# Kernel tuning notes

Measured on AMD Instinct MI355X. Metric: run time of the kernel, lower is better.

## Reference

```python
import jax, jax.numpy as jnp
import numpy as np

B, S, H = 4, 2048, 1024
NH = 1                     # source code only type-checks with 1 head (see notes)
DH = H // NH               # head dim == hidden size
DT = 32                    # distance_type
LN_EPS = 1e-12


def setup_inputs() -> dict:
    key = jax.random.key(0)
    ks = jax.random.split(key, 12)
    sd = 0.02
    hidden_states = jax.random.normal(ks[0], (B, S, H), dtype=jnp.float32)
    attention_mask = jnp.zeros((B, 1, 1, S), dtype=jnp.float32)
    word_word_relation = jax.random.randint(ks[1], (B, S, S), 0, DT, dtype=jnp.int64)
    dist_emb = sd * jax.random.normal(ks[2], (DT, H), dtype=jnp.float32)
    dist_emb = dist_emb.at[0].set(0.0)  # padding_idx=0
    return {
        "hidden_states": hidden_states,
        "attention_mask": attention_mask,
        "word_word_relation": word_word_relation,
        "Wq": sd * jax.random.normal(ks[3], (H, H), dtype=jnp.float32),
        "bq": jnp.zeros((H,), dtype=jnp.float32),
        "Wk": sd * jax.random.normal(ks[4], (H, H), dtype=jnp.float32),
        "bk": jnp.zeros((H,), dtype=jnp.float32),
        "Wv": sd * jax.random.normal(ks[5], (H, H), dtype=jnp.float32),
        "bv": jnp.zeros((H,), dtype=jnp.float32),
        "dist_emb": dist_emb,
        "Wo": sd * jax.random.normal(ks[6], (H, H), dtype=jnp.float32),
        "bo": jnp.zeros((H,), dtype=jnp.float32),
        "ln_g": jnp.ones((H,), dtype=jnp.float32),
        "ln_b": jnp.zeros((H,), dtype=jnp.float32),
    }


def _split_heads(x):
    # [B,S,H] -> [B,NH,S,DH]
    return x.reshape(B, S, NH, DH).transpose(0, 2, 1, 3)


def reference(hidden_states, attention_mask, word_word_relation, Wq, bq, Wk, bk,
              Wv, bv, dist_emb, Wo, bo, ln_g, ln_b):
    q = _split_heads(hidden_states @ Wq.T + bq)   # [B,NH,S,DH]
    k = _split_heads(hidden_states @ Wk.T + bk)
    v = _split_heads(hidden_states @ Wv.T + bv)

    # raw QK^T scores [B,NH,S,S]
    scores = jnp.einsum('bhqd,bhkd->bhqk', q, k)

    # query . distance_embedding^T : [B,NH,S,DT]
    word_dot_distance = jnp.einsum('bhqd,td->bhqt', q, dist_emb)

    rel = word_word_relation[:, None, :, :]       # [B,1,S,S]
    # gather per-pair distance score along the distance-type axis
    dist_att = jnp.take_along_axis(word_dot_distance, rel, axis=3)  # [B,NH,S,S]
    mask_out = (rel == 1).astype(scores.dtype)    # keep only relation==1 pairs
    dist_att = dist_att * mask_out

    scores = (scores + dist_att) / jnp.sqrt(jnp.asarray(DH, scores.dtype))
    scores = scores + attention_mask              # additive BERT mask
    probs = jax.nn.softmax(scores, axis=-1)       # dropout p=0 -> identity

    ctx = jnp.einsum('bhqk,bhkd->bhqd', probs, v) # [B,NH,S,DH]
    ctx = ctx.transpose(0, 2, 1, 3).reshape(B, S, H)

    # BertSelfOutput: dense -> residual -> LayerNorm
    attn_out = ctx @ Wo.T + bo
    x = attn_out + hidden_states
    mu = jnp.mean(x, axis=-1, keepdims=True)
    var = jnp.mean(jnp.square(x - mu), axis=-1, keepdims=True)
    out = (x - mu) * jax.lax.rsqrt(var + LN_EPS) * ln_g + ln_b
    return out
```

## Files before the change

### kernel.cpp

```cpp
#include <hip/hip_runtime.h>

#define BM 256
#define BN 128
#define BK 64
#define NBUF 3
#define BUFELEMS ((BM + BN) * BK)

typedef __bf16 bf16x8 __attribute__((ext_vector_type(8)));
typedef __bf16 bf16x4 __attribute__((ext_vector_type(4)));
typedef float f32x4 __attribute__((ext_vector_type(4)));
typedef __bf16 bf16_t;

#define MFMA16(a, b, c) __builtin_amdgcn_mfma_f32_16x16x32_bf16((a), (b), (c), 0, 0, 0)

__device__ __forceinline__ void gl_lds16(const void* g, void* l) {
    __builtin_amdgcn_global_load_lds(
        (const __attribute__((address_space(1))) void*)g,
        (__attribute__((address_space(3))) void*)l, 16, 0, 0);
}
__device__ __forceinline__ void barrier_mem() {
    asm volatile("s_barrier" ::: "memory");
}

__global__ __launch_bounds__(256)
void cvt_all_kernel(const float* __restrict__ hid,
                    const float* __restrict__ w0, const float* __restrict__ w1,
                    const float* __restrict__ w2, const float* __restrict__ w3,
                    bf16_t* __restrict__ hidb, bf16_t* __restrict__ wb)
{
    const int bid = blockIdx.x;
    const float* src;
    bf16_t* dst;
    size_t off;
    if (bid < 8192) {
        src = hid; dst = hidb; off = (size_t)bid * 1024;
    } else {
        const int i = (bid - 8192) >> 10;
        src = (i == 0) ? w0 : (i == 1) ? w1 : (i == 2) ? w2 : w3;
        dst = wb + (size_t)i * 1024 * 1024;
        off = (size_t)((bid - 8192) & 1023) * 1024;
    }
    const size_t idx = off + threadIdx.x * 4;
    const float4 v = *(const float4*)(src + idx);
    bf16x4 o;
    o[0] = (__bf16)v.x; o[1] = (__bf16)v.y;
    o[2] = (__bf16)v.z; o[3] = (__bf16)v.w;
    *(bf16x4*)(dst + idx) = o;
}

#define PHASE(BUF, P, SG, SL, VM)                                            \
  do {                                                                       \
    bf16x8 a00 = rdA(BUF, 2 * (P), 0),     a01 = rdA(BUF, 2 * (P), 1);       \
    bf16x8 a10 = rdA(BUF, 2 * (P) + 1, 0), a11 = rdA(BUF, 2 * (P) + 1, 1);   \
    if ((P) == 0) {                                                          \
      _Pragma("unroll")                                                      \
      for (int nf = 0; nf < 4; ++nf) {                                       \
        bfrag[nf][0] = rdB(BUF, nf, 0);                                      \
        bfrag[nf][1] = rdB(BUF, nf, 1);                                      \
      }                                                                      \
    }                                                                        \
    if (SG) {                                                                \
      gl_lds16((SG) + soff,                   (SL) + (w << 9));              \
      gl_lds16((SG) + soff + (size_t)64 * K,  (SL) + 4096 + (w << 9));       \
    }                                                                        \
    barrier_mem();                                                           \
    asm volatile("s_waitcnt lgkmcnt(0)" ::: "memory");                       \
    __builtin_amdgcn_s_setprio(1);                                           \
    _Pragma("unroll")                                                        \
    for (int nf = 0; nf < 4; ++nf) {                                         \
      acc[2 * (P)][nf]     = MFMA16(a00, bfrag[nf][0], acc[2 * (P)][nf]);    \
      acc[2 * (P)][nf]     = MFMA16(a01, bfrag[nf][1], acc[2 * (P)][nf]);    \
      acc[2 * (P) + 1][nf] = MFMA16(a10, bfrag[nf][0], acc[2 * (P) + 1][nf]);\
      acc[2 * (P) + 1][nf] = MFMA16(a11, bfrag[nf][1], acc[2 * (P) + 1][nf]);\
    }                                                                        \
    __builtin_amdgcn_s_setprio(0);                                           \
    if ((VM) == 4)      asm volatile("s_waitcnt vmcnt(4)" ::: "memory");     \
    else if ((VM) == 0) asm volatile("s_waitcnt vmcnt(0)" ::: "memory");     \
    barrier_mem();                                                           \
  } while (0)

template <int MODE>
__global__ __launch_bounds__(512, 2)
void gemm8(const bf16_t* __restrict__ A, const bf16_t* __restrict__ Bw,
           const float* __restrict__ bias, const float* __restrict__ bias2,
           const float* __restrict__ bias3,
           bf16_t* __restrict__ C, bf16_t* __restrict__ C2,
           int M, int N, int K,
           long long sAz, long long sBz, long long sCz,
           int Sdim, int DHdim)
{
    const int bz = blockIdx.z;
    const float* bi = bias;
    if (MODE == 0) {
        Bw += (long long)bz * N * K;
        bi = (bz == 0) ? bias : (bz == 1 ? bias2 : bias3);
        if (bz < 2) C += (long long)bz * sCz;
    } else {
        A += (long long)bz * sAz;
        Bw += (long long)bz * sBz;
        C += (long long)bz * sCz;
    }
    const int num_n = N >> 8;
    const int pid = blockIdx.x;
    const int group = 8 * num_n;
    const int g = pid / group;
    const int m0 = (g * 8 + (pid % 8)) * 256;
    const int n0 = ((pid % group) >> 3) * 256;

    const int tid = threadIdx.x;
    const int w = tid >> 6;
    const int lane = tid & 63;
    const int wr = w >> 2;
    const int wc = w & 3;
    const int frow = lane & 15;
    const int fchunk = lane >> 4;

    __shared__ bf16_t smem[4 * 16384];
    bf16_t* A0b = smem;
    bf16_t* A1b = smem + 16384;
    bf16_t* B0b = smem + 32768;
    bf16_t* B1b = smem + 49152;

    const int srow = tid >> 3;
    const int sch  = (tid & 7) ^ (srow & 7);
    const size_t soff = (size_t)srow * K + ((size_t)sch << 3);

    const bf16_t* gA = A + (size_t)m0 * K;
    const bf16_t* gB = Bw + (size_t)n0 * K;

    auto rdA = [&](int buf, int mf, int kh) -> bf16x8 {
        const int row = wr * 128 + mf * 16 + frow;
        return *(const bf16x8*)&smem[buf * 16384 + row * 64 +
                                     (((kh * 4 + fchunk) ^ (frow & 7)) << 3)];
    };
    auto rdB = [&](int buf, int nf, int kh) -> bf16x8 {
        const int row = wc * 64 + nf * 16 + frow;
        return *(const bf16x8*)&smem[32768 + buf * 16384 + row * 64 +
                                     (((kh * 4 + fchunk) ^ (frow & 7)) << 3)];
    };
    auto issue = [&](const bf16_t* sg, bf16_t* sl) {
        gl_lds16(sg + soff,                  sl + (w << 9));
        gl_lds16(sg + soff + (size_t)64 * K, sl + 4096 + (w << 9));
    };

    f32x4 acc[8][4];
#pragma unroll
    for (int i = 0; i < 8; ++i)
#pragma unroll
        for (int j = 0; j < 4; ++j) acc[i][j] = (f32x4)0.0f;
    bf16x8 bfrag[4][2];

    const int NT = K >> 6;
    const int NI = NT >> 1;

    issue(gB,                       B0b);
    issue(gB + (size_t)128 * K,     B0b + 8192);
    issue(gA,                       A0b);
    issue(gA + (size_t)128 * K,     A0b + 8192);
    issue(gB + 64,                  B1b);
    issue(gB + 64 + (size_t)128 * K, B1b + 8192);
    asm volatile("s_waitcnt vmcnt(4)" ::: "memory");
    barrier_mem();

    for (int it = 0; it < NI; ++it) {
        const int t0 = 2 * it;
        const bool pf = (t0 + 2) < NT;
        const bf16_t* a1g = gA + (size_t)(t0 + 1) * 64;
        const bf16_t* a2g = pf ? gA + (size_t)(t0 + 2) * 64 : nullptr;
        const bf16_t* b2g = pf ? gB + (size_t)(t0 + 2) * 64 : nullptr;
        const bf16_t* b3g = pf ? gB + (size_t)(t0 + 3) * 64 : nullptr;

        PHASE(0, 0, a1g,                                      A1b,        -1);
        PHASE(0, 1, a1g + (size_t)128 * K,                    A1b + 8192, -1);
        PHASE(0, 2, b2g,                                      B0b,        -1);
        PHASE(0, 3, (b2g ? b2g + (size_t)128 * K : nullptr),  B0b + 8192, (pf ? 4 : 0));
        PHASE(1, 0, a2g,                                      A0b,        -1);
        PHASE(1, 1, (a2g ? a2g + (size_t)128 * K : nullptr),  A0b + 8192, -1);
        PHASE(1, 2, b3g,                                      B1b,        -1);
        PHASE(1, 3, (b3g ? b3g + (size_t)128 * K : nullptr),  B1b + 8192, (pf ? 4 : -1));
    }

    const int crow = (lane >> 4) * 4;
    const int ccol = lane & 15;

    if (MODE == 0 && bz == 2) {
#pragma unroll
        for (int mt = 0; mt < 8; ++mt) {
            const int mb = m0 + wr * 128 + mt * 16 + crow;
#pragma unroll
            for (int nt = 0; nt < 4; ++nt) {
                const int n = n0 + wc * 64 + nt * 16 + ccol;
                const float bvv = bi[n];
                const int b = mb >> 11;
                const int s = mb & 2047;
                union { ushort4 u; bf16_t h[4]; } pk;
#pragma unroll
                for (int r = 0; r < 4; ++r) pk.h[r] = (__bf16)(acc[mt][nt][r] + bvv);
                *(ushort4*)&C2[(size_t)b * DHdim * Sdim + (size_t)n * Sdim + s] = pk.u;
            }
        }
        return;
    }

    bf16_t* tw = smem + w * (16 * 72);
    const int r0 = lane >> 3;
    const int cseg = (lane & 7) * 8;

    float bv[4];
    if (MODE == 0) {
#pragma unroll
        for (int nt = 0; nt < 4; ++nt)
            bv[nt] = bi[n0 + wc * 64 + nt * 16 + ccol];
    }

#pragma unroll
    for (int mt = 0; mt < 8; ++mt) {
#pragma unroll
        for (int nt = 0; nt < 4; ++nt) {
            const float badd = (MODE == 0) ? bv[nt] : 0.0f;
#pragma unroll
            for (int r = 0; r < 4; ++r)
                tw[(crow + r) * 72 + nt * 16 + ccol] = (__bf16)(acc[mt][nt][r] + badd);
        }
        bf16x8 va = *(const bf16x8*)&tw[r0 * 72 + cseg];
        bf16x8 vb = *(const bf16x8*)&tw[(r0 + 8) * 72 + cseg];
        const int gm_a = m0 + wr * 128 + mt * 16 + r0;
        const int gm_b = gm_a + 8;
        const int gn = n0 + wc * 64 + cseg;
        *(bf16x8*)&C[(size_t)gm_a * N + gn] = va;
        *(bf16x8*)&C[(size_t)gm_b * N + gn] = vb;
    }
}

template <int MODE>
__global__ __launch_bounds__(512, 2)
void gemm_bt(const bf16_t* __restrict__ A, const bf16_t* __restrict__ Bw,
             const float* __restrict__ bias, const float* __restrict__ bias2,
             const float* __restrict__ bias3,
             bf16_t* __restrict__ C, bf16_t* __restrict__ C2,
             int M, int N, int K,
             long long sAz, long long sBz, long long sCz,
             const float* __restrict__ resid,
             int Sdim, int DHdim)
{
    const int bz = blockIdx.z;
    const float* bi = bias;
    if (MODE == 0) {
        Bw += (long long)bz * N * K;
        bi = (bz == 0) ? bias : (bz == 1 ? bias2 : bias3);
        if (bz < 2) C += (long long)bz * sCz;
    } else {
        A += (long long)bz * sAz;
        Bw += (long long)bz * sBz;
        C += (long long)bz * sCz;
    }
    const int num_n = N / BN;
    const int pid = blockIdx.x;
    const int group = 8 * num_n;
    const int g = pid / group;
    const int m0 = (g * 8 + (pid % 8)) * BM;
    const int n0 = ((pid % group) >> 3) * BN;

    const int tid = threadIdx.x;
    const int w = tid >> 6;
    const int lane = tid & 63;
    const int wr = w >> 1;
    const int wc = w & 1;
    const int frow = lane & 15;
    const int fchunk = lane >> 4;

    __shared__ bf16_t smem[NBUF * BUFELEMS];

    const int srow8 = lane >> 3;
    const int sch = (lane & 7) ^ srow8;
    const size_t soff = (size_t)(w * 8 + srow8) * K + ((size_t)sch << 3);
    const bf16_t* gA = A + (size_t)m0 * K;
    const bf16_t* gB = Bw + (size_t)n0 * K;

    auto stA = [&](int kt, int b, int i) {
        gl_lds16(gA + (size_t)(i * 64) * K + (size_t)kt * BK + soff,
                 smem + (size_t)b * BUFELEMS + (i * 64 + w * 8) * BK);
    };
    auto stB = [&](int kt, int b, int i) {
        gl_lds16(gB + (size_t)(i * 64) * K + (size_t)kt * BK + soff,
                 smem + (size_t)b * BUFELEMS + BM * BK + (i * 64 + w * 8) * BK);
    };

    f32x4 acc[4][4];
#pragma unroll
    for (int i = 0; i < 4; ++i)
#pragma unroll
        for (int j = 0; j < 4; ++j) acc[i][j] = (f32x4)0.0f;

    const int NT = K / BK;

#pragma unroll
    for (int i = 0; i < 4; ++i) stA(0, 0, i);
#pragma unroll
    for (int i = 0; i < 2; ++i) stB(0, 0, i);
#pragma unroll
    for (int i = 0; i < 4; ++i) stA(1, 1, i);
#pragma unroll
    for (int i = 0; i < 2; ++i) stB(1, 1, i);

    for (int kt = 0; kt < NT; ++kt) {
        const int cur = kt % NBUF;
        const int nxt = (kt + 2) % NBUF;
        const bool pf = (kt + 2 < NT);
        if (pf) { stA(kt + 2, nxt, 0); stA(kt + 2, nxt, 1); stA(kt + 2, nxt, 2); }
        if (pf)               asm volatile("s_waitcnt vmcnt(9)" ::: "memory");
        else if (kt + 1 < NT) asm volatile("s_waitcnt vmcnt(6)" ::: "memory");
        else                  asm volatile("s_waitcnt vmcnt(0)" ::: "memory");
        barrier_mem();

        const bf16_t* Ab = smem + (size_t)cur * BUFELEMS;
        const bf16_t* Bb = Ab + BM * BK;
        const int sw = frow & 7;

        bf16x8 af[4], b0v[2][2];
#pragma unroll
        for (int t = 0; t < 4; ++t) {
            const int row = wr * 64 + t * 16 + frow;
            af[t] = *(const bf16x8*)&Ab[row * BK + ((fchunk ^ sw) << 3)];
        }
        bf16x8 af1[4];
#pragma unroll
        for (int t = 0; t < 4; ++t) {
            const int row = wr * 64 + t * 16 + frow;
            af1[t] = *(const bf16x8*)&Ab[row * BK + (((4 + fchunk) ^ sw) << 3)];
        }
#pragma unroll
        for (int u = 0; u < 2; ++u) {
            const int row = wc * 64 + u * 16 + frow;
#pragma unroll
            for (int kh = 0; kh < 2; ++kh)
                b0v[u][kh] = *(const bf16x8*)&Bb[row * BK + (((kh * 4 + fchunk) ^ sw) << 3)];
        }
        if (pf) { stA(kt + 2, nxt, 3); stB(kt + 2, nxt, 0); stB(kt + 2, nxt, 1); }

        __builtin_amdgcn_s_setprio(1);
#pragma unroll
        for (int t = 0; t < 4; ++t)
#pragma unroll
            for (int u = 0; u < 2; ++u) {
                acc[t][u] = MFMA16(af[t], b0v[u][0], acc[t][u]);
                acc[t][u] = MFMA16(af1[t], b0v[u][1], acc[t][u]);
            }
        __builtin_amdgcn_s_setprio(0);

        bf16x8 b1v[2][2];
#pragma unroll
        for (int u = 0; u < 2; ++u) {
            const int row = wc * 64 + (u + 2) * 16 + frow;
#pragma unroll
            for (int kh = 0; kh < 2; ++kh)
                b1v[u][kh] = *(const bf16x8*)&Bb[row * BK + (((kh * 4 + fchunk) ^ sw) << 3)];
        }
        barrier_mem();

        __builtin_amdgcn_s_setprio(1);
#pragma unroll
        for (int t = 0; t < 4; ++t)
#pragma unroll
            for (int u = 0; u < 2; ++u) {
                acc[t][u + 2] = MFMA16(af[t], b1v[u][0], acc[t][u + 2]);
                acc[t][u + 2] = MFMA16(af1[t], b1v[u][1], acc[t][u + 2]);
            }
        __builtin_amdgcn_s_setprio(0);
        barrier_mem();
    }

    const int crow = (lane >> 4) * 4;
    const int ccol = lane & 15;

    bf16_t* tw = smem + w * (16 * 72);
    const int r0 = lane >> 3;
    const int cseg = (lane & 7) * 8;

    float bv[4];
    if (MODE == 4) {
#pragma unroll
        for (int nt = 0; nt < 4; ++nt)
            bv[nt] = bi[n0 + wc * 64 + nt * 16 + ccol];
    }

#pragma unroll
    for (int mt = 0; mt < 4; ++mt) {
#pragma unroll
        for (int nt = 0; nt < 4; ++nt) {
            const float badd = (MODE == 4) ? bv[nt] : 0.0f;
#pragma unroll
            for (int r = 0; r < 4; ++r)
                tw[(crow + r) * 72 + nt * 16 + ccol] = (__bf16)(acc[mt][nt][r] + badd);
        }
        bf16x8 va = *(const bf16x8*)&tw[r0 * 72 + cseg];
        bf16x8 vb = *(const bf16x8*)&tw[(r0 + 8) * 72 + cseg];

        const int gm_a = m0 + wr * 64 + mt * 16 + r0;
        const int gm_b = gm_a + 8;
        const int gn = n0 + wc * 64 + cseg;

        if (MODE == 3) {
            *(bf16x8*)&C[(size_t)gm_a * N + gn] = va;
            *(bf16x8*)&C[(size_t)gm_b * N + gn] = vb;
        } else {
            const float4 xa0 = *(const float4*)&resid[(size_t)gm_a * N + gn];
            const float4 xa1 = *(const float4*)&resid[(size_t)gm_a * N + gn + 4];
            const float4 xb0 = *(const float4*)&resid[(size_t)gm_b * N + gn];
            const float4 xb1 = *(const float4*)&resid[(size_t)gm_b * N + gn + 4];
            bf16x8 oa, ob;
            oa[0] = (__bf16)((float)va[0] + xa0.x);
            oa[1] = (__bf16)((float)va[1] + xa0.y);
            oa[2] = (__bf16)((float)va[2] + xa0.z);
            oa[3] = (__bf16)((float)va[3] + xa0.w);
            oa[4] = (__bf16)((float)va[4] + xa1.x);
            oa[5] = (__bf16)((float)va[5] + xa1.y);
            oa[6] = (__bf16)((float)va[6] + xa1.z);
            oa[7] = (__bf16)((float)va[7] + xa1.w);
            ob[0] = (__bf16)((float)vb[0] + xb0.x);
            ob[1] = (__bf16)((float)vb[1] + xb0.y);
            ob[2] = (__bf16)((float)vb[2] + xb0.z);
            ob[3] = (__bf16)((float)vb[3] + xb0.w);
            ob[4] = (__bf16)((float)vb[4] + xb1.x);
            ob[5] = (__bf16)((float)vb[5] + xb1.y);
            ob[6] = (__bf16)((float)vb[6] + xb1.z);
            ob[7] = (__bf16)((float)vb[7] + xb1.w);
            *(bf16x8*)&C[(size_t)gm_a * N + gn] = oa;
            *(bf16x8*)&C[(size_t)gm_b * N + gn] = ob;
        }
    }
}

__global__ __launch_bounds__(256)
void softmax_kernel(bf16_t* __restrict__ sc, const int* __restrict__ rel,
                    const bf16_t* __restrict__ q, const float* __restrict__ de,
                    const float* __restrict__ mask)
{
    constexpr int S = 2048, H = 1024;
    const int row = blockIdx.x;
    const int b = row >> 11;
    const int tid = threadIdx.x;
    const int w = tid >> 6, lane = tid & 63;
    __shared__ float rd1[4], rmax[4], rsum[4];

    const bf16x4 q4 = *(const bf16x4*)(q + (size_t)row * H + tid * 4);
    const float4 e4 = *(const float4*)(de + H + tid * 4);
    float pd = (float)q4[0] * e4.x + (float)q4[1] * e4.y
             + (float)q4[2] * e4.z + (float)q4[3] * e4.w;
#pragma unroll
    for (int off = 32; off; off >>= 1) pd += __shfl_xor(pd, off, 64);
    if (lane == 0) rd1[w] = pd;
    __syncthreads();
    const float d1s = (rd1[0] + rd1[1] + rd1[2] + rd1[3]) * 0.03125f;

    bf16_t* p = sc + (size_t)row * S;
    const bf16x8 x = *(const bf16x8*)(p + tid * 8);
    const int4 rl0 = *(const int4*)&rel[(size_t)row * S + tid * 8];
    const int4 rl1 = *(const int4*)&rel[(size_t)row * S + tid * 8 + 4];
    const float4 mk0 = *(const float4*)&mask[(size_t)b * S + tid * 8];
    const float4 mk1 = *(const float4*)&mask[(size_t)b * S + tid * 8 + 4];
    const int rls[8] = {rl0.x, rl0.y, rl0.z, rl0.w, rl1.x, rl1.y, rl1.z, rl1.w};
    const float mks[8] = {mk0.x, mk0.y, mk0.z, mk0.w, mk1.x, mk1.y, mk1.z, mk1.w};
    float v[8];
    float mx = -1e30f;
#pragma unroll
    for (int j = 0; j < 8; ++j) {
        v[j] = (float)x[j] * 0.03125f + mks[j] + (rls[j] == 1 ? d1s : 0.0f);
        mx = fmaxf(mx, v[j]);
    }
#pragma unroll
    for (int off = 32; off; off >>= 1) mx = fmaxf(mx, __shfl_xor(mx, off, 64));
    if (lane == 0) rmax[w] = mx;
    __syncthreads();
    mx = fmaxf(fmaxf(rmax[0], rmax[1]), fmaxf(rmax[2], rmax[3]));
    float sum = 0.0f;
#pragma unroll
    for (int j = 0; j < 8; ++j) { v[j] = __expf(v[j] - mx); sum += v[j]; }
#pragma unroll
    for (int off = 32; off; off >>= 1) sum += __shfl_xor(sum, off, 64);
    if (lane == 0) rsum[w] = sum;
    __syncthreads();
    sum = rsum[0] + rsum[1] + rsum[2] + rsum[3];
    const float inv = 1.0f / sum;
    bf16x8 o;
#pragma unroll
    for (int j = 0; j < 8; ++j) o[j] = (__bf16)(v[j] * inv);
    *(bf16x8*)(p + tid * 8) = o;
}

__global__ __launch_bounds__(256)
void ln_kernel(const bf16_t* __restrict__ x, const float* __restrict__ gamma,
               const float* __restrict__ beta, float* __restrict__ out)
{
    const int H = 1024;
    const size_t row = blockIdx.x;
    const int tid = threadIdx.x;
    const int w = tid >> 6, lane = tid & 63;
    bf16x4 xv = *(const bf16x4*)(x + row * H + tid * 4);
    float v[4] = {(float)xv[0], (float)xv[1], (float)xv[2], (float)xv[3]};
    float s = 0.0f, s2 = 0.0f;
#pragma unroll
    for (int j = 0; j < 4; ++j) { s += v[j]; s2 += v[j] * v[j]; }
#pragma unroll
    for (int off = 32; off; off >>= 1) {
        s += __shfl_xor(s, off, 64);
        s2 += __shfl_xor(s2, off, 64);
    }
    __shared__ float rs[4], rs2[4];
    if (lane == 0) { rs[w] = s; rs2[w] = s2; }
    __syncthreads();
    s  = rs[0] + rs[1] + rs[2] + rs[3];
    s2 = rs2[0] + rs2[1] + rs2[2] + rs2[3];
    const float mu  = s * (1.0f / H);
    const float var = s2 * (1.0f / H) - mu * mu;
    const float inv = rsqrtf(var + 1e-12f);
    float4 o;
    const int c = tid * 4;
    o.x = (v[0] - mu) * inv * gamma[c + 0] + beta[c + 0];
    o.y = (v[1] - mu) * inv * gamma[c + 1] + beta[c + 1];
    o.z = (v[2] - mu) * inv * gamma[c + 2] + beta[c + 2];
    o.w = (v[3] - mu) * inv * gamma[c + 3] + beta[c + 3];
    *(float4*)(out + row * H + tid * 4) = o;
}

extern "C" void kernel_launch(void* const* d_in, const int* in_sizes, int n_in,
                              void* d_out, int out_size, void* d_ws, size_t ws_size,
                              hipStream_t stream)
{
    constexpr int B = 4, S = 2048, H = 1024;
    const float* hid = (const float*)d_in[0];
    const float* am  = (const float*)d_in[1];
    const int*   rel = (const int*)d_in[2];
    const float* Wq  = (const float*)d_in[3];
    const float* bq  = (const float*)d_in[4];
    const float* Wk  = (const float*)d_in[5];
    const float* bk  = (const float*)d_in[6];
    const float* Wv  = (const float*)d_in[7];
    const float* bv  = (const float*)d_in[8];
    const float* de  = (const float*)d_in[9];
    const float* Wo  = (const float*)d_in[10];
    const float* bo  = (const float*)d_in[11];
    const float* lng = (const float*)d_in[12];
    const float* lnb = (const float*)d_in[13];
    float* out = (float*)d_out;

    char* ws = (char*)d_ws;
    const int n_tok = B * S;
    const size_t MB = 1024 * 1024;
    bf16_t* hidb = (bf16_t*)(ws);
    bf16_t* Wqb  = (bf16_t*)(ws + 16 * MB);
    bf16_t* Wob  = (bf16_t*)(ws + 22 * MB);
    bf16_t* qb   = (bf16_t*)(ws + 24 * MB);
    bf16_t* kb   = (bf16_t*)(ws + 40 * MB);
    bf16_t* vT   = (bf16_t*)(ws + 56 * MB);
    bf16_t* ctx  = (bf16_t*)(ws + 72 * MB);
    bf16_t* sc   = (bf16_t*)(ws + 88 * MB);
    bf16_t* xb   = (bf16_t*)(ws + 88 * MB);

    const dim3 blk(256);
    const dim3 blkg(512);
    cvt_all_kernel<<<dim3(8192 + 4 * 1024), blk, 0, stream>>>(
        hid, Wq, Wk, Wv, Wo, hidb, Wqb);

    gemm8<0><<<dim3(32 * 4, 1, 3), blkg, 0, stream>>>(
        hidb, Wqb, bq, bk, bv, qb, vT, n_tok, H, H,
        0, 0, (long long)n_tok * H, S, H);
    gemm8<3><<<dim3(8 * 8, 1, B), blkg, 0, stream>>>(
        qb, kb, nullptr, nullptr, nullptr, sc, nullptr, S, S, H,
        (long long)S * H, (long long)S * H, (long long)S * S, S, H);
    softmax_kernel<<<dim3(B * S), blk, 0, stream>>>(sc, rel, qb, de, am);
    gemm_bt<3><<<dim3((S / BM) * (H / BN), 1, B), blkg, 0, stream>>>(
        sc, vT, nullptr, nullptr, nullptr, ctx, nullptr, S, H, S,
        (long long)S * S, (long long)H * S, (long long)S * H,
        nullptr, S, H);
    gemm_bt<4><<<dim3((n_tok / BM) * (H / BN), 1, 1), blkg, 0, stream>>>(
        ctx, Wob, bo, nullptr, nullptr, xb, nullptr, n_tok, H, H, 0, 0, 0,
        hid, S, H);
    ln_kernel<<<dim3(n_tok), blk, 0, stream>>>(xb, lng, lnb, out);
}
```

Baseline: 339.5 us.

## Restructure GEMM mainloop into K-half quarter phases with split LDS buffers

Reorganizes the bf16 GEMM main loop so each 64-wide K tile is split into two 32-wide halves stored in separate LDS regions. The loop now runs four quarter-phases per tile with new prefetch and vmcnt scheduling. Each phase loads fragments from one K-half and issues a half-tile async load. The XOR swizzle is dropped for a plain 32-element row layout, which may introduce LDS bank conflicts in exchange for simpler addressing and finer-grained overlap.

```diff
diff --git a/kernel.cpp b/kernel.cpp
--- a/kernel.cpp
+++ b/kernel.cpp
@@ -48,35 +48,34 @@
     *(bf16x4*)(dst + idx) = o;
 }
 
-#define PHASE(BUF, P, SG, SL, VM)                                            \
-  do {                                                                       \
-    bf16x8 a00 = rdA(BUF, 2 * (P), 0),     a01 = rdA(BUF, 2 * (P), 1);       \
-    bf16x8 a10 = rdA(BUF, 2 * (P) + 1, 0), a11 = rdA(BUF, 2 * (P) + 1, 1);   \
-    if ((P) == 0) {                                                          \
-      _Pragma("unroll")                                                      \
-      for (int nf = 0; nf < 4; ++nf) {                                       \
-        bfrag[nf][0] = rdB(BUF, nf, 0);                                      \
-        bfrag[nf][1] = rdB(BUF, nf, 1);                                      \
-      }                                                                      \
-    }                                                                        \
-    if (SG) {                                                                \
-      gl_lds16((SG) + soff,                   (SL) + (w << 9));              \
-      gl_lds16((SG) + soff + (size_t)64 * K,  (SL) + 4096 + (w << 9));       \
-    }                                                                        \
-    barrier_mem();                                                           \
-    asm volatile("s_waitcnt lgkmcnt(0)" ::: "memory");                       \
-    __builtin_amdgcn_s_setprio(1);                                           \
-    _Pragma("unroll")                                                        \
-    for (int nf = 0; nf < 4; ++nf) {                                         \
-      acc[2 * (P)][nf]     = MFMA16(a00, bfrag[nf][0], acc[2 * (P)][nf]);    \
-      acc[2 * (P)][nf]     = MFMA16(a01, bfrag[nf][1], acc[2 * (P)][nf]);    \
-      acc[2 * (P) + 1][nf] = MFMA16(a10, bfrag[nf][0], acc[2 * (P) + 1][nf]);\
-      acc[2 * (P) + 1][nf] = MFMA16(a11, bfrag[nf][1], acc[2 * (P) + 1][nf]);\
-    }                                                                        \
-    __builtin_amdgcn_s_setprio(0);                                           \
-    if ((VM) == 4)      asm volatile("s_waitcnt vmcnt(4)" ::: "memory");     \
-    else if ((VM) == 0) asm volatile("s_waitcnt vmcnt(0)" ::: "memory");     \
-    barrier_mem();                                                           \
+#define ABASE(b, k) (((b) * 2 + (k)) * 8192)
+#define BBASE(b, k) (32768 + ((b) * 2 + (k)) * 8192)
+
+#define QP(BUF, MH, KH, RDB, DOST, SRC, DST, VM)                              \
+  do {                                                                        \
+    if ((VM) == 8)      asm volatile("s_waitcnt vmcnt(8)" ::: "memory");      \
+    else if ((VM) == 4) asm volatile("s_waitcnt vmcnt(4)" ::: "memory");      \
+    else if ((VM) == 0) asm volatile("s_waitcnt vmcnt(0)" ::: "memory");      \
+    barrier_mem();                                                            \
+    bf16x8 af0 = rdA(BUF, KH, (MH) * 4 + 0);                                  \
+    bf16x8 af1 = rdA(BUF, KH, (MH) * 4 + 1);                                  \
+    bf16x8 af2 = rdA(BUF, KH, (MH) * 4 + 2);                                  \
+    bf16x8 af3 = rdA(BUF, KH, (MH) * 4 + 3);                                  \
+    if (RDB) {                                                                \
+      bfr[0] = rdB(BUF, KH, 0); bfr[1] = rdB(BUF, KH, 1);                     \
+      bfr[2] = rdB(BUF, KH, 2); bfr[3] = rdB(BUF, KH, 3);                     \
+    }                                                                         \
+    if (DOST) issueHalf((SRC), (DST));                                        \
+    asm volatile("s_waitcnt lgkmcnt(0)" ::: "memory");                        \
+    __builtin_amdgcn_s_setprio(1);                                            \
+    _Pragma("unroll")                                                         \
+    for (int nf = 0; nf < 4; ++nf) {                                          \
+      acc[(MH) * 4 + 0][nf] = MFMA16(af0, bfr[nf], acc[(MH) * 4 + 0][nf]);    \
+      acc[(MH) * 4 + 1][nf] = MFMA16(af1, bfr[nf], acc[(MH) * 4 + 1][nf]);    \
+      acc[(MH) * 4 + 2][nf] = MFMA16(af2, bfr[nf], acc[(MH) * 4 + 2][nf]);    \
+      acc[(MH) * 4 + 3][nf] = MFMA16(af3, bfr[nf], acc[(MH) * 4 + 3][nf]);    \
+    }                                                                         \
+    __builtin_amdgcn_s_setprio(0);                                            \
   } while (0)
 
 template <int MODE>
@@ -115,32 +114,24 @@
     const int frow = lane & 15;
     const int fchunk = lane >> 4;
 
-    __shared__ bf16_t smem[4 * 16384];
-    bf16_t* A0b = smem;
-    bf16_t* A1b = smem + 16384;
-    bf16_t* B0b = smem + 32768;
-    bf16_t* B1b = smem + 49152;
-
-    const int srow = tid >> 3;
-    const int sch  = (tid & 7) ^ (srow & 7);
-    const size_t soff = (size_t)srow * K + ((size_t)sch << 3);
+    __shared__ bf16_t smem[8 * 8192];
+
+    const size_t soff = (size_t)(tid >> 2) * K + (size_t)(tid & 3) * 8;
 
     const bf16_t* gA = A + (size_t)m0 * K;
     const bf16_t* gB = Bw + (size_t)n0 * K;
 
-    auto rdA = [&](int buf, int mf, int kh) -> bf16x8 {
+    auto rdA = [&](int buf, int kh, int mf) -> bf16x8 {
         const int row = wr * 128 + mf * 16 + frow;
-        return *(const bf16x8*)&smem[buf * 16384 + row * 64 +
-                                     (((kh * 4 + fchunk) ^ (frow & 7)) << 3)];
+        return *(const bf16x8*)&smem[ABASE(buf, kh) + row * 32 + fchunk * 8];
     };
-    auto rdB = [&](int buf, int nf, int kh) -> bf16x8 {
+    auto rdB = [&](int buf, int kh, int nf) -> bf16x8 {
         const int row = wc * 64 + nf * 16 + frow;
-        return *(const bf16x8*)&smem[32768 + buf * 16384 + row * 64 +
-                                     (((kh * 4 + fchunk) ^ (frow & 7)) << 3)];
+        return *(const bf16x8*)&smem[BBASE(buf, kh) + row * 32 + fchunk * 8];
     };
-    auto issue = [&](const bf16_t* sg, bf16_t* sl) {
-        gl_lds16(sg + soff,                  sl + (w << 9));
-        gl_lds16(sg + soff + (size_t)64 * K, sl + 4096 + (w << 9));
+    auto issueHalf = [&](const bf16_t* src, int dst) {
+        gl_lds16(src + soff,                   smem + dst + (w << 9));
+        gl_lds16(src + (size_t)128 * K + soff, smem + dst + 4096 + (w << 9));
     };
 
     f32x4 acc[8][4];
@@ -148,37 +139,37 @@
     for (int i = 0; i < 8; ++i)
 #pragma unroll
         for (int j = 0; j < 4; ++j) acc[i][j] = (f32x4)0.0f;
-    bf16x8 bfrag[4][2];
+    bf16x8 bfr[4];
 
     const int NT = K >> 6;
-    const int NI = NT >> 1;
-
-    issue(gB,                       B0b);
-    issue(gB + (size_t)128 * K,     B0b + 8192);
-    issue(gA,                       A0b);
-    issue(gA + (size_t)128 * K,     A0b + 8192);
-    issue(gB + 64,                  B1b);
-    issue(gB + 64 + (size_t)128 * K, B1b + 8192);
-    asm volatile("s_waitcnt vmcnt(4)" ::: "memory");
+
+    issueHalf(gA,      ABASE(0, 0));
+    issueHalf(gB,      BBASE(0, 0));
+    issueHalf(gA + 32, ABASE(0, 1));
+    issueHalf(gB + 32, BBASE(0, 1));
+    issueHalf(gA + 64, ABASE(1, 0));
+    issueHalf(gB + 64, BBASE(1, 0));
+
+    for (int t = 0; t < NT; ++t) {
+        const int buf = t & 1;
+        const bool s1 = (t + 1 < NT);
+        const bool s2 = (t + 2 < NT);
+        const bf16_t* aS1 = gA + (size_t)(t + 1) * 64 + 32;
+        const bf16_t* bS1 = gB + (size_t)(t + 1) * 64 + 32;
+        const bf16_t* aS2 = gA + (size_t)(t + 2) * 64;
+        const bf16_t* bS2 = gB + (size_t)(t + 2) * 64;
+        const int dA1 = ABASE((t + 1) & 1, 1);
+        const int dB1 = BBASE((t + 1) & 1, 1);
+        const int dA2 = ABASE(t & 1, 0);
+        const int dB2 = BBASE(t & 1, 0);
+        const int vq1 = (t == NT - 1) ? 4 : 8;
+        const int vq3 = (t == NT - 1) ? 0 : 8;
+        QP(buf, 0, 0, 1, s1, aS1, dA1, vq1);
+        QP(buf, 1, 0, 0, s1, bS1, dB1, -1);
+        QP(buf, 0, 1, 1, s2, aS2, dA2, vq3);
+        QP(buf, 1, 1, 0, s2, bS2, dB2, -1);
+    }
     barrier_mem();
-
-    for (int it = 0; it < NI; ++it) {
-        const int t0 = 2 * it;
-        const bool pf = (t0 + 2) < NT;
-        const bf16_t* a1g = gA + (size_t)(t0 + 1) * 64;
-        const bf16_t* a2g = pf ? gA + (size_t)(t0 + 2) * 64 : nullptr;
-        const bf16_t* b2g = pf ? gB + (size_t)(t0 + 2) * 64 : nullptr;
-        const bf16_t* b3g = pf ? gB + (size_t)(t0 + 3) * 64 : nullptr;
-
-        PHASE(0, 0, a1g,                                      A1b,        -1);
-        PHASE(0, 1, a1g + (size_t)128 * K,                    A1b + 8192, -1);
-        PHASE(0, 2, b2g,                                      B0b,        -1);
-        PHASE(0, 3, (b2g ? b2g + (size_t)128 * K : nullptr),  B0b + 8192, (pf ? 4 : 0));
-        PHASE(1, 0, a2g,                                      A0b,        -1);
-        PHASE(1, 1, (a2g ? a2g + (size_t)128 * K : nullptr),  A0b + 8192, -1);
-        PHASE(1, 2, b3g,                                      B1b,        -1);
-        PHASE(1, 3, (b3g ? b3g + (size_t)128 * K : nullptr),  B1b + 8192, (pf ? 4 : -1));
-    }
 
     const int crow = (lane >> 4) * 4;
     const int ccol = lane & 15;
```

New measurement: 343.6 us. Within noise of the previous version (+1.2%).
